# Kernel tuning notes

Hardware: AMD Instinct MI355X
Metric: run time of the kernel (lower is better)

The kernel has to match this reference:

```python
import jax, jax.numpy as jnp
import numpy as np

N_NODES = 100000
N_EDGES = 3200000
NFEAT = 128
NHID = 128
NCLASS = 8
BN_EPS = 1e-5


def setup_inputs() -> dict:
    key = jax.random.key(0)
    ks = jax.random.split(key, 8)
    x = jax.random.normal(ks[0], (N_NODES, NFEAT), dtype=jnp.float32)
    edge_index = jax.random.randint(ks[1], (2, N_EDGES), 0, N_NODES, dtype=jnp.int64)
    # GCNConv params: weight [nfeat, nhid] (glorot), bias [nhid]
    lim = float(np.sqrt(6.0 / (NFEAT + NHID)))
    W = jax.random.uniform(ks[2], (NFEAT, NHID), minval=-lim, maxval=lim, dtype=jnp.float32)
    b_gc = jnp.zeros((NHID,), dtype=jnp.float32)
    # BatchNorm1d params
    gamma = jnp.ones((NHID,), dtype=jnp.float32)
    beta = jnp.zeros((NHID,), dtype=jnp.float32)
    # fc head: (nhid/2) -> nclass, xavier_uniform, zero bias
    lim2 = float(np.sqrt(6.0 / (NHID // 2 + NCLASS)))
    fc_w = jax.random.uniform(ks[3], (NCLASS, NHID // 2), minval=-lim2, maxval=lim2, dtype=jnp.float32)
    fc_b = jnp.zeros((NCLASS,), dtype=jnp.float32)
    return {"x": x, "edge_index": edge_index, "W": W, "b_gc": b_gc,
            "gamma": gamma, "beta": beta, "fc_w": fc_w, "fc_b": fc_b}


def _gcn_conv(x, edge_index, W, b):
    """PyG GCNConv: add self-loops, symmetric norm, linear, gather-scatter, bias."""
    N = x.shape[0]
    loops = jnp.arange(N, dtype=edge_index.dtype)
    src = jnp.concatenate([edge_index[0], loops])  # source (row / x_j)
    dst = jnp.concatenate([edge_index[1], loops])  # target (col / aggregation index)
    # degree of target nodes (edge weight = 1)
    deg = jax.ops.segment_sum(jnp.ones_like(dst, dtype=x.dtype), dst, num_segments=N)
    dinv = jnp.where(deg > 0, jax.lax.rsqrt(deg), 0.0)
    norm = dinv[src] * dinv[dst]  # [E+N]
    h = x @ W  # [N, nhid]
    msg = h[src] * norm[:, None]  # gather + scale
    out = jax.ops.segment_sum(msg, dst, num_segments=N)  # scatter-add
    return out + b


def _batchnorm(h, gamma, beta):
    mean = jnp.mean(h, axis=0)
    var = jnp.mean(jnp.square(h - mean), axis=0)  # biased, training-mode
    return gamma * (h - mean) * jax.lax.rsqrt(var + BN_EPS) + beta


def reference(x, edge_index, W, b_gc, gamma, beta, fc_w, fc_b):
    h = _gcn_conv(x, edge_index, W, b_gc)
    embed = _batchnorm(h, gamma, beta)
    half = embed.shape[1] // 2
    out = embed[:, :half] @ fc_w.T + fc_b
    return (out, embed)
```

## Files before the change

kernel.cpp:

```cpp
#include <hip/hip_runtime.h>
#include <hip/hip_bf16.h>
#include <math.h>

#define N_NODES 100000
#define N_EDGES 3200000
#define NFEAT 128
#define NHID 128
#define NCLASS 8
#define BN_EPS 1e-5f
#define CB 512
#define NBC 196
#define EPB 8192
#define PART_BLOCKS 391
#define WT_BLOCKS 64

typedef __attribute__((ext_vector_type(8))) short short8;
typedef __attribute__((ext_vector_type(4))) float f32x4;

__device__ __forceinline__ short f2bf(float f) {
    __hip_bfloat16 b = __float2bfloat16(f);
    return *reinterpret_cast<short*>(&b);
}
__device__ __forceinline__ float bf_lo(unsigned u) { return __uint_as_float(u << 16); }
__device__ __forceinline__ float bf_hi(unsigned u) { return __uint_as_float(u & 0xffff0000u); }


__global__ __launch_bounds__(256) void k_chist(const int* __restrict__ dst,
                                               int* __restrict__ ghist,
                                               const float* __restrict__ W,
                                               unsigned short* __restrict__ Wt,
                                               uint4* __restrict__ hbz) {
    if (blockIdx.x >= PART_BLOCKS) {
        int idx = (blockIdx.x - PART_BLOCKS) * 256 + threadIdx.x;
        if (idx < 16) hbz[idx] = (uint4){0u, 0u, 0u, 0u};
        int k = idx >> 7, n = idx & 127;
        Wt[n * NFEAT + k] = (unsigned short)f2bf(W[idx]);
        return;
    }
    __shared__ int lh[NBC];
    const int tid = threadIdx.x;
    if (tid < NBC) lh[tid] = 0;
    __syncthreads();
    const int4* dst4 = (const int4*)dst;
    const int q0 = blockIdx.x * (EPB / 4) + tid;
#pragma unroll
    for (int i = 0; i < 8; ++i) {
        int q = q0 + i * 256;
        if (q < N_EDGES / 4) {
            int4 d = dst4[q];
            atomicAdd(&lh[d.x >> 9], 1);
            atomicAdd(&lh[d.y >> 9], 1);
            atomicAdd(&lh[d.z >> 9], 1);
            atomicAdd(&lh[d.w >> 9], 1);
        }
    }
    __syncthreads();
    if (tid < NBC) {
        int c = lh[tid];
        if (c) atomicAdd(&ghist[tid], c);
    }
}

__global__ __launch_bounds__(512) void k_cscan(const int* __restrict__ ghist,
                                               int* __restrict__ coff,
                                               int* __restrict__ ccur,
                                               int* __restrict__ off,
                                               float* __restrict__ stats,
                                               int* __restrict__ ticket) {
    __shared__ int tmp[512];
    const int t = threadIdx.x;
    if (t < 256) stats[t] = 0.f;
    if (t == 0) *ticket = 0;
    int v = (t < NBC) ? ghist[t] : 0;
    tmp[t] = v;
    __syncthreads();
    for (int d = 1; d < 512; d <<= 1) {
        int u = (t >= d) ? tmp[t - d] : 0;
        __syncthreads();
        tmp[t] += u;
        __syncthreads();
    }
    int excl = tmp[t] - v;
    if (t < NBC) {
        coff[t] = excl;
        ccur[t] = excl;
    }
    if (t == NBC - 1) {
        coff[NBC] = tmp[t];
        off[N_NODES] = tmp[t];
    }
}


__global__ __launch_bounds__(256) void k_part(const int* __restrict__ src,
                                              const int* __restrict__ dst,
                                              int* __restrict__ ccur,
                                              unsigned* __restrict__ epack) {
    __shared__ int lh[NBC];
    __shared__ int lstart[NBC];
    __shared__ int adj[NBC];
    __shared__ int stmp[256];
    __shared__ unsigned sorted[EPB];
    __shared__ unsigned short bkt[EPB];
    const int tid = threadIdx.x;
    if (tid < NBC) lh[tid] = 0;
    __syncthreads();
    const int4* src4 = (const int4*)src;
    const int4* dst4 = (const int4*)dst;
    const int q0 = blockIdx.x * (EPB / 4) + tid;
    int4 sv[8], dv[8];
    int rk[32];
#pragma unroll
    for (int i = 0; i < 8; ++i) {
        int q = q0 + i * 256;
        if (q < N_EDGES / 4) {
            sv[i] = src4[q];
            dv[i] = dst4[q];
            rk[i * 4 + 0] = atomicAdd(&lh[dv[i].x >> 9], 1);
            rk[i * 4 + 1] = atomicAdd(&lh[dv[i].y >> 9], 1);
            rk[i * 4 + 2] = atomicAdd(&lh[dv[i].z >> 9], 1);
            rk[i * 4 + 3] = atomicAdd(&lh[dv[i].w >> 9], 1);
        } else dv[i].x = -1;
    }
    __syncthreads();
    int v = (tid < NBC) ? lh[tid] : 0;
    stmp[tid] = v;
    __syncthreads();
    for (int d = 1; d < 256; d <<= 1) {
        int u = (tid >= d) ? stmp[tid - d] : 0;
        __syncthreads();
        stmp[tid] += u;
        __syncthreads();
    }
    if (tid < NBC) {
        int ls = stmp[tid] - v;
        lstart[tid] = ls;
        adj[tid] = (v ? atomicAdd(&ccur[tid], v) : 0) - ls;
    }
    __syncthreads();
#pragma unroll
    for (int i = 0; i < 8; ++i) {
        if (dv[i].x >= 0) {
            int b, p;
            b = dv[i].x >> 9; p = lstart[b] + rk[i * 4 + 0];
            sorted[p] = ((unsigned)sv[i].x << 9) | (unsigned)(dv[i].x & 511); bkt[p] = (unsigned short)b;
            b = dv[i].y >> 9; p = lstart[b] + rk[i * 4 + 1];
            sorted[p] = ((unsigned)sv[i].y << 9) | (unsigned)(dv[i].y & 511); bkt[p] = (unsigned short)b;
            b = dv[i].z >> 9; p = lstart[b] + rk[i * 4 + 2];
            sorted[p] = ((unsigned)sv[i].z << 9) | (unsigned)(dv[i].z & 511); bkt[p] = (unsigned short)b;
            b = dv[i].w >> 9; p = lstart[b] + rk[i * 4 + 3];
            sorted[p] = ((unsigned)sv[i].w << 9) | (unsigned)(dv[i].w & 511); bkt[p] = (unsigned short)b;
        }
    }
    __syncthreads();
    const int vcnt = stmp[255];
    for (int p = tid; p < vcnt; p += 256)
        epack[p + adj[bkt[p]]] = sorted[p];
}


__global__ __launch_bounds__(256) void k_fine(const unsigned* __restrict__ epack,
                                              const int* __restrict__ coff,
                                              int* __restrict__ off,
                                              float* __restrict__ dinv,
                                              int* __restrict__ esrc) {
    __shared__ int lh[CB], lcur[CB], lsc[256];
    const int tid = threadIdx.x;
    const int b = blockIdx.x;
    const int node0 = b << 9;
    lh[tid] = 0;
    lh[tid + 256] = 0;
    __syncthreads();
    const int lo = coff[b], hiEnd = coff[b + 1];
    for (int i = lo + tid; i < hiEnd; i += 256)
        atomicAdd(&lh[epack[i] & 511u], 1);
    __syncthreads();
    int v0 = lh[2 * tid], v1 = lh[2 * tid + 1];
    int s = v0 + v1;
    lsc[tid] = s;
    __syncthreads();
    for (int d = 1; d < 256; d <<= 1) {
        int u = (tid >= d) ? lsc[tid - d] : 0;
        __syncthreads();
        lsc[tid] += u;
        __syncthreads();
    }
    int pairExcl = lsc[tid] - s;
    lcur[2 * tid] = pairExcl;
    lcur[2 * tid + 1] = pairExcl + v0;
    int n0 = node0 + 2 * tid, n1 = n0 + 1;
    if (n0 < N_NODES) { off[n0] = lo + pairExcl;      dinv[n0] = rsqrtf((float)(v0 + 1)); }
    if (n1 < N_NODES) { off[n1] = lo + pairExcl + v0; dinv[n1] = rsqrtf((float)(v1 + 1)); }
    __syncthreads();
    for (int i = lo + tid; i < hiEnd; i += 256) {
        unsigned p = epack[i];
        int pos = atomicAdd(&lcur[p & 511u], 1);
        esrc[lo + pos] = (int)(p >> 9);
    }
}


#define WSTRIDE 136
__global__ __launch_bounds__(256) void k_gemm(const float* __restrict__ x,
                                              const unsigned short* __restrict__ Wt,
                                              const float* __restrict__ dinv,
                                              unsigned short* __restrict__ hb) {
    __shared__ short wlds[NHID * WSTRIDE];
    const int tid = threadIdx.x;

    const unsigned* Wt32 = (const unsigned*)Wt;
    unsigned* wl32 = (unsigned*)wlds;
#pragma unroll
    for (int i = 0; i < 32; ++i) {
        int d = tid + i * 256;
        int n = d >> 6, kp = d & 63;
        wl32[n * (WSTRIDE / 2) + kp] = Wt32[d];
    }
    __syncthreads();

    const int wid = tid >> 6, lane = tid & 63;
    const int qw = lane >> 4, lr = lane & 15;
    const int arow = blockIdx.x * 64 + wid * 16 + lr;
    const bool avalid = arow < N_NODES;

    short8 a[4];
#pragma unroll
    for (int ks = 0; ks < 4; ++ks) {
        if (avalid) {
            const float* p = x + (size_t)arow * NFEAT + ks * 32 + qw * 8;
            float4 v0 = *(const float4*)p;
            float4 v1 = *(const float4*)(p + 4);
            short8 t;
            t[0] = f2bf(v0.x); t[1] = f2bf(v0.y); t[2] = f2bf(v0.z); t[3] = f2bf(v0.w);
            t[4] = f2bf(v1.x); t[5] = f2bf(v1.y); t[6] = f2bf(v1.z); t[7] = f2bf(v1.w);
            a[ks] = t;
        } else {
            short8 t;
#pragma unroll
            for (int j = 0; j < 8; ++j) t[j] = 0;
            a[ks] = t;
        }
    }

    f32x4 acc[8];
#pragma unroll
    for (int nt = 0; nt < 8; ++nt) acc[nt] = (f32x4){0.f, 0.f, 0.f, 0.f};

#pragma unroll
    for (int nt = 0; nt < 8; ++nt) {
#pragma unroll
        for (int ks = 0; ks < 4; ++ks) {
            short8 bfr = *(const short8*)&wlds[(nt * 16 + lr) * WSTRIDE + ks * 32 + qw * 8];
            acc[nt] = __builtin_amdgcn_mfma_f32_16x16x32_bf16(a[ks], bfr, acc[nt], 0, 0, 0);
        }
    }

    const int rbase = blockIdx.x * 64 + wid * 16 + qw * 4;
    float dv[4];
#pragma unroll
    for (int j = 0; j < 4; ++j) dv[j] = (rbase + j < N_NODES) ? dinv[rbase + j] : 0.f;
#pragma unroll
    for (int j = 0; j < 4; ++j) {
        int r = rbase + j;
        if (r >= N_NODES) continue;
#pragma unroll
        for (int nt = 0; nt < 8; ++nt)
            hb[(size_t)r * NHID + nt * 16 + lr] = (unsigned short)f2bf(dv[j] * acc[nt][j]);
    }
}


__global__ __launch_bounds__(256) void k_agg(const int* __restrict__ off,
                                             const int* __restrict__ esrc,
                                             const float* __restrict__ dinv,
                                             const uint2* __restrict__ hbq,
                                             float4* __restrict__ agg4) {
    const int node = (blockIdx.x << 2) | (threadIdx.x >> 6);
    const int lane = threadIdx.x & 63;
    const int hl = lane >> 5;
    const int cl = lane & 31;
    if (node >= N_NODES) return;

    const float dn = dinv[node];
    const int self = hl ? N_NODES : node;
    uint2 u0 = hbq[(size_t)self * 32 + cl];
    float aAx = bf_lo(u0.x), aAy = bf_hi(u0.x), aAz = bf_lo(u0.y), aAw = bf_hi(u0.y);
    float aBx = 0.f, aBy = 0.f, aBz = 0.f, aBw = 0.f;
    float aCx = 0.f, aCy = 0.f, aCz = 0.f, aCw = 0.f;
    float aDx = 0.f, aDy = 0.f, aDz = 0.f, aDw = 0.f;

    const int begin = off[node], end = off[node + 1];
    for (int base = begin; base < end; base += 64) {
        int m = end - base;
        if (m > 64) m = 64;
        int sv = (lane < m) ? esrc[base + lane] : N_NODES;
        const int kmax = (m + 7) >> 3;
        for (int k = 0; k < kmax; ++k) {
            int sA = __shfl(sv, 8 * k + 0 + hl);
            int sB = __shfl(sv, 8 * k + 2 + hl);
            int sC = __shfl(sv, 8 * k + 4 + hl);
            int sD = __shfl(sv, 8 * k + 6 + hl);
            uint2 uA = hbq[(size_t)sA * 32 + cl];
            uint2 uB = hbq[(size_t)sB * 32 + cl];
            uint2 uC = hbq[(size_t)sC * 32 + cl];
            uint2 uD = hbq[(size_t)sD * 32 + cl];
            aAx += bf_lo(uA.x); aAy += bf_hi(uA.x); aAz += bf_lo(uA.y); aAw += bf_hi(uA.y);
            aBx += bf_lo(uB.x); aBy += bf_hi(uB.x); aBz += bf_lo(uB.y); aBw += bf_hi(uB.y);
            aCx += bf_lo(uC.x); aCy += bf_hi(uC.x); aCz += bf_lo(uC.y); aCw += bf_hi(uC.y);
            aDx += bf_lo(uD.x); aDy += bf_hi(uD.x); aDz += bf_lo(uD.y); aDw += bf_hi(uD.y);
        }
    }
    float ax = (aAx + aBx) + (aCx + aDx);
    float ay = (aAy + aBy) + (aCy + aDy);
    float az = (aAz + aBz) + (aCz + aDz);
    float aw = (aAw + aBw) + (aCw + aDw);
    ax += __shfl_xor(ax, 32);
    ay += __shfl_xor(ay, 32);
    az += __shfl_xor(az, 32);
    aw += __shfl_xor(aw, 32);
    if (hl == 0) {
        float4 o;
        o.x = ax * dn; o.y = ay * dn; o.z = az * dn; o.w = aw * dn;
        agg4[(size_t)node * 32 + cl] = o;
    }
}


__global__ __launch_bounds__(256) void k_stats(const float* __restrict__ agg,
                                               float* __restrict__ stats,
                                               int* __restrict__ ticket,
                                               const float* __restrict__ gamma,
                                               const float* __restrict__ beta,
                                               float* __restrict__ ss) {
    const int cb = threadIdx.x & 31;
    const int rg = threadIdx.x >> 5;
    const float4* a4 = (const float4*)agg;
    float4 s = {0.f, 0.f, 0.f, 0.f}, s2 = {0.f, 0.f, 0.f, 0.f};
    for (int r = blockIdx.x * 8 + rg; r < N_NODES; r += gridDim.x * 8) {
        float4 v = a4[(size_t)r * 32 + cb];
        s.x += v.x; s.y += v.y; s.z += v.z; s.w += v.w;
        s2.x += v.x * v.x; s2.y += v.y * v.y; s2.z += v.z * v.z; s2.w += v.w * v.w;
    }
    __shared__ float4 ls[256], ls2[256];
    __shared__ int lastflag;
    ls[threadIdx.x] = s;
    ls2[threadIdx.x] = s2;
    __syncthreads();
    if (rg == 0) {
        float4 ts = ls[cb], t2 = ls2[cb];
#pragma unroll
        for (int g = 1; g < 8; ++g) {
            float4 v = ls[g * 32 + cb], w = ls2[g * 32 + cb];
            ts.x += v.x; ts.y += v.y; ts.z += v.z; ts.w += v.w;
            t2.x += w.x; t2.y += w.y; t2.z += w.z; t2.w += w.w;
        }
        atomicAdd(&stats[cb * 4 + 0], ts.x);
        atomicAdd(&stats[cb * 4 + 1], ts.y);
        atomicAdd(&stats[cb * 4 + 2], ts.z);
        atomicAdd(&stats[cb * 4 + 3], ts.w);
        atomicAdd(&stats[128 + cb * 4 + 0], t2.x);
        atomicAdd(&stats[128 + cb * 4 + 1], t2.y);
        atomicAdd(&stats[128 + cb * 4 + 2], t2.z);
        atomicAdd(&stats[128 + cb * 4 + 3], t2.w);
    }
    __threadfence();
    __syncthreads();
    if (threadIdx.x == 0)
        lastflag = (atomicAdd(ticket, 1) == (int)gridDim.x - 1) ? 1 : 0;
    __syncthreads();
    if (lastflag && threadIdx.x < NHID) {
        int c = threadIdx.x;
        float sum = atomicAdd(&stats[c], 0.f);
        float sq  = atomicAdd(&stats[128 + c], 0.f);
        float mean = sum / (float)N_NODES;
        float var = fmaxf(sq / (float)N_NODES - mean * mean, 0.f);
        float inv = rsqrtf(var + BN_EPS);
        float sc = gamma[c] * inv;
        ss[c] = sc;
        ss[128 + c] = beta[c] - mean * sc;
    }
}


__global__ __launch_bounds__(256) void k_bnfc(float* __restrict__ embed,
                                              const float* __restrict__ ss,
                                              const float* __restrict__ fc_w,
                                              const float* __restrict__ fc_b,
                                              float* __restrict__ out) {
    __shared__ float se[64][68];
    __shared__ float sw[8][68];
    __shared__ float sb[8];
    const int tid = threadIdx.x;
    const int row0 = blockIdx.x * 64;
    {
        int d = tid;
        sw[d >> 6][d & 63] = fc_w[d];
        d = tid + 256;
        sw[d >> 6][d & 63] = fc_w[d];
        if (tid < 8) sb[tid] = fc_b[tid];
    }
    float4* ef4 = (float4*)embed;
    const float4* ssc4 = (const float4*)ss;
    const float4* ssh4 = (const float4*)(ss + 128);
#pragma unroll
    for (int i = 0; i < 8; ++i) {
        int d = tid + i * 256;
        int r = d >> 5;
        int cb = d & 31;
        int gr = row0 + r;
        if (gr < N_NODES) {
            float4 v = ef4[(size_t)gr * 32 + cb];
            float4 sc = ssc4[cb], sh = ssh4[cb];
            v.x = fmaf(v.x, sc.x, sh.x);
            v.y = fmaf(v.y, sc.y, sh.y);
            v.z = fmaf(v.z, sc.z, sh.z);
            v.w = fmaf(v.w, sc.w, sh.w);
            ef4[(size_t)gr * 32 + cb] = v;
            if (cb < 16) {
                se[r][cb * 4 + 0] = v.x; se[r][cb * 4 + 1] = v.y;
                se[r][cb * 4 + 2] = v.z; se[r][cb * 4 + 3] = v.w;
            }
        } else if (cb < 16) {
            se[r][cb * 4 + 0] = 0.f; se[r][cb * 4 + 1] = 0.f;
            se[r][cb * 4 + 2] = 0.f; se[r][cb * 4 + 3] = 0.f;
        }
    }
    __syncthreads();
    const int r = tid >> 2;
    const int j0 = (tid & 3) * 2;
    const int gr = row0 + r;
#pragma unroll
    for (int jj = 0; jj < 2; ++jj) {
        int j = j0 + jj;
        float s = sb[j];
#pragma unroll
        for (int k = 0; k < 64; ++k) s = fmaf(se[r][k], sw[j][k], s);
        if (gr < N_NODES) out[(size_t)gr * NCLASS + j] = s;
    }
}


extern "C" void kernel_launch(void* const* d_in, const int* in_sizes, int n_in,
                              void* d_out, int out_size, void* d_ws, size_t ws_size,
                              hipStream_t stream) {
    const float* x     = (const float*)d_in[0];
    const int*   ei    = (const int*)d_in[1];
    const float* W     = (const float*)d_in[2];
    const float* gamma = (const float*)d_in[4];
    const float* beta  = (const float*)d_in[5];
    const float* fc_w  = (const float*)d_in[6];
    const float* fc_b  = (const float*)d_in[7];

    const int* src = ei;
    const int* dst = ei + N_EDGES;

    float* out   = (float*)d_out;
    float* embed = (float*)d_out + (size_t)N_NODES * NCLASS;

    char* ws = (char*)d_ws;
    size_t o = 0;
    unsigned* epack = (unsigned*)(ws + o);          o += (size_t)N_EDGES * 4;
    unsigned short* hb = (unsigned short*)(ws + o); o += (size_t)(N_NODES + 1) * NHID * 2;
    o = (o + 255) & ~(size_t)255;
    int* esrc   = (int*)(ws + o);                   o += (size_t)N_EDGES * 4;
    int* off    = (int*)(ws + o);                   o += (size_t)(N_NODES + 1) * 4;
    float* dinv = (float*)(ws + o);                 o += (size_t)N_NODES * 4;
    unsigned short* Wt = (unsigned short*)(ws + o); o += (size_t)NFEAT * NHID * 2;
    float* stats = (float*)(ws + o);                o += 256 * 4;
    float* ss    = (float*)(ws + o);                o += 256 * 4;
    int* ghist   = (int*)(ws + o);                  o += NBC * 4;
    int* coff    = (int*)(ws + o);                  o += (NBC + 1) * 4;
    int* ccur    = (int*)(ws + o);                  o += NBC * 4;
    int* ticket  = (int*)(ws + o);                  o += 4;

    hipMemsetAsync(ghist, 0, NBC * 4, stream);

    k_chist<<<PART_BLOCKS + WT_BLOCKS, 256, 0, stream>>>(dst, ghist, W, Wt,
                                                         (uint4*)(hb + (size_t)N_NODES * NHID));
    k_cscan<<<1, 512, 0, stream>>>(ghist, coff, ccur, off, stats, ticket);
    k_part<<<PART_BLOCKS, 256, 0, stream>>>(src, dst, ccur, epack);
    k_fine<<<NBC, 256, 0, stream>>>(epack, coff, off, dinv, esrc);

    k_gemm<<<(N_NODES + 63) / 64, 256, 0, stream>>>(x, Wt, dinv, hb);

    k_agg<<<(N_NODES + 3) / 4, 256, 0, stream>>>(off, esrc, dinv, (const uint2*)hb, (float4*)embed);

    k_stats<<<512, 256, 0, stream>>>(embed, stats, ticket, gamma, beta, ss);

    k_bnfc<<<(N_NODES + 63) / 64, 256, 0, stream>>>(embed, ss, fc_w, fc_b, out);
}
```

Baseline: 314.3 us.

## Fuse BN statistics into aggregation kernel and stage x through LDS in GEMM

The aggregation kernel becomes persistent-style, with 2048 blocks looping over groups of four nodes. It accumulates per-column sums and sums of squares while writing each output row, then reduces them per block and does the last-block ticket finalize, so the separate stats kernel and its re-read of the 100000x128 fp32 buffer go away. The GEMM now loads x tiles into padded LDS with coalesced float4 loads before forming MFMA fragments, in place of per-lane strided global loads. In exchange the aggregation grid is smaller, which may reduce latency hiding for the irregular gathers, and the GEMM uses more shared memory per block.

```diff
diff --git a/kernel.cpp b/kernel.cpp
--- a/kernel.cpp
+++ b/kernel.cpp
@@ -13,6 +13,8 @@
 #define EPB 8192
 #define PART_BLOCKS 391
 #define WT_BLOCKS 64
+#define AGG_BLOCKS 2048
+#define NODE_GROUPS (N_NODES / 4)
 
 typedef __attribute__((ext_vector_type(8))) short short8;
 typedef __attribute__((ext_vector_type(4))) float f32x4;
@@ -201,12 +203,15 @@
 
 
 #define WSTRIDE 136
+#define XSTRIDE 136
 __global__ __launch_bounds__(256) void k_gemm(const float* __restrict__ x,
                                               const unsigned short* __restrict__ Wt,
                                               const float* __restrict__ dinv,
                                               unsigned short* __restrict__ hb) {
-    __shared__ short wlds[NHID * WSTRIDE];
+    __shared__ __align__(16) short wlds[NHID * WSTRIDE];
+    __shared__ __align__(16) short xl[64 * XSTRIDE];
     const int tid = threadIdx.x;
+    const int row0 = blockIdx.x * 64;
 
     const unsigned* Wt32 = (const unsigned*)Wt;
     unsigned* wl32 = (unsigned*)wlds;
@@ -216,31 +221,27 @@
         int n = d >> 6, kp = d & 63;
         wl32[n * (WSTRIDE / 2) + kp] = Wt32[d];
     }
+    const float4* x4 = (const float4*)x;
+#pragma unroll
+    for (int i = 0; i < 8; ++i) {
+        int idx = tid + i * 256;
+        int r = idx >> 5, c4 = idx & 31;
+        int gr = row0 + r;
+        float4 vv = (gr < N_NODES) ? x4[(size_t)gr * 32 + c4]
+                                   : (float4){0.f, 0.f, 0.f, 0.f};
+        short4 t;
+        t.x = f2bf(vv.x); t.y = f2bf(vv.y); t.z = f2bf(vv.z); t.w = f2bf(vv.w);
+        *(short4*)&xl[r * XSTRIDE + c4 * 4] = t;
+    }
     __syncthreads();
 
     const int wid = tid >> 6, lane = tid & 63;
     const int qw = lane >> 4, lr = lane & 15;
-    const int arow = blockIdx.x * 64 + wid * 16 + lr;
-    const bool avalid = arow < N_NODES;
 
     short8 a[4];
 #pragma unroll
-    for (int ks = 0; ks < 4; ++ks) {
-        if (avalid) {
-            const float* p = x + (size_t)arow * NFEAT + ks * 32 + qw * 8;
-            float4 v0 = *(const float4*)p;
-            float4 v1 = *(const float4*)(p + 4);
-            short8 t;
-            t[0] = f2bf(v0.x); t[1] = f2bf(v0.y); t[2] = f2bf(v0.z); t[3] = f2bf(v0.w);
-            t[4] = f2bf(v1.x); t[5] = f2bf(v1.y); t[6] = f2bf(v1.z); t[7] = f2bf(v1.w);
-            a[ks] = t;
-        } else {
-            short8 t;
-#pragma unroll
-            for (int j = 0; j < 8; ++j) t[j] = 0;
-            a[ks] = t;
-        }
-    }
+    for (int ks = 0; ks < 4; ++ks)
+        a[ks] = *(const short8*)&xl[(wid * 16 + lr) * XSTRIDE + ks * 32 + qw * 8];
 
     f32x4 acc[8];
 #pragma unroll
@@ -274,99 +275,95 @@
                                              const int* __restrict__ esrc,
                                              const float* __restrict__ dinv,
                                              const uint2* __restrict__ hbq,
-                                             float4* __restrict__ agg4) {
-    const int node = (blockIdx.x << 2) | (threadIdx.x >> 6);
+                                             float4* __restrict__ agg4,
+                                             float* __restrict__ stats,
+                                             int* __restrict__ ticket,
+                                             const float* __restrict__ gamma,
+                                             const float* __restrict__ beta,
+                                             float* __restrict__ ss) {
+    const int wv = threadIdx.x >> 6;
     const int lane = threadIdx.x & 63;
     const int hl = lane >> 5;
     const int cl = lane & 31;
-    if (node >= N_NODES) return;
-
-    const float dn = dinv[node];
-    const int self = hl ? N_NODES : node;
-    uint2 u0 = hbq[(size_t)self * 32 + cl];
-    float aAx = bf_lo(u0.x), aAy = bf_hi(u0.x), aAz = bf_lo(u0.y), aAw = bf_hi(u0.y);
-    float aBx = 0.f, aBy = 0.f, aBz = 0.f, aBw = 0.f;
-    float aCx = 0.f, aCy = 0.f, aCz = 0.f, aCw = 0.f;
-    float aDx = 0.f, aDy = 0.f, aDz = 0.f, aDw = 0.f;
-
-    const int begin = off[node], end = off[node + 1];
-    for (int base = begin; base < end; base += 64) {
-        int m = end - base;
-        if (m > 64) m = 64;
-        int sv = (lane < m) ? esrc[base + lane] : N_NODES;
-        const int kmax = (m + 7) >> 3;
-        for (int k = 0; k < kmax; ++k) {
-            int sA = __shfl(sv, 8 * k + 0 + hl);
-            int sB = __shfl(sv, 8 * k + 2 + hl);
-            int sC = __shfl(sv, 8 * k + 4 + hl);
-            int sD = __shfl(sv, 8 * k + 6 + hl);
-            uint2 uA = hbq[(size_t)sA * 32 + cl];
-            uint2 uB = hbq[(size_t)sB * 32 + cl];
-            uint2 uC = hbq[(size_t)sC * 32 + cl];
-            uint2 uD = hbq[(size_t)sD * 32 + cl];
-            aAx += bf_lo(uA.x); aAy += bf_hi(uA.x); aAz += bf_lo(uA.y); aAw += bf_hi(uA.y);
-            aBx += bf_lo(uB.x); aBy += bf_hi(uB.x); aBz += bf_lo(uB.y); aBw += bf_hi(uB.y);
-            aCx += bf_lo(uC.x); aCy += bf_hi(uC.x); aCz += bf_lo(uC.y); aCw += bf_hi(uC.y);
-            aDx += bf_lo(uD.x); aDy += bf_hi(uD.x); aDz += bf_lo(uD.y); aDw += bf_hi(uD.y);
-        }
-    }
-    float ax = (aAx + aBx) + (aCx + aDx);
-    float ay = (aAy + aBy) + (aCy + aDy);
-    float az = (aAz + aBz) + (aCz + aDz);
-    float aw = (aAw + aBw) + (aCw + aDw);
-    ax += __shfl_xor(ax, 32);
-    ay += __shfl_xor(ay, 32);
-    az += __shfl_xor(az, 32);
-    aw += __shfl_xor(aw, 32);
+
+    float4 sAcc = {0.f, 0.f, 0.f, 0.f}, qAcc = {0.f, 0.f, 0.f, 0.f};
+
+    for (int ng = blockIdx.x; ng < NODE_GROUPS; ng += AGG_BLOCKS) {
+        const int node = ng * 4 + wv;
+        const float dn = dinv[node];
+        const int self = hl ? N_NODES : node;
+        uint2 u0 = hbq[(size_t)self * 32 + cl];
+        float aAx = bf_lo(u0.x), aAy = bf_hi(u0.x), aAz = bf_lo(u0.y), aAw = bf_hi(u0.y);
+        float aBx = 0.f, aBy = 0.f, aBz = 0.f, aBw = 0.f;
+        float aCx = 0.f, aCy = 0.f, aCz = 0.f, aCw = 0.f;
+        float aDx = 0.f, aDy = 0.f, aDz = 0.f, aDw = 0.f;
+
+        const int begin = off[node], end = off[node + 1];
+        for (int base = begin; base < end; base += 64) {
+            int m = end - base;
+            if (m > 64) m = 64;
+            int sv = (lane < m) ? esrc[base + lane] : N_NODES;
+            const int kmax = (m + 7) >> 3;
+            for (int k = 0; k < kmax; ++k) {
+                int sA = __shfl(sv, 8 * k + 0 + hl);
+                int sB = __shfl(sv, 8 * k + 2 + hl);
+                int sC = __shfl(sv, 8 * k + 4 + hl);
+                int sD = __shfl(sv, 8 * k + 6 + hl);
+                uint2 uA = hbq[(size_t)sA * 32 + cl];
+                uint2 uB = hbq[(size_t)sB * 32 + cl];
+                uint2 uC = hbq[(size_t)sC * 32 + cl];
+                uint2 uD = hbq[(size_t)sD * 32 + cl];
+                aAx += bf_lo(uA.x); aAy += bf_hi(uA.x); aAz += bf_lo(uA.y); aAw += bf_hi(uA.y);
+                aBx += bf_lo(uB.x); aBy += bf_hi(uB.x); aBz += bf_lo(uB.y); aBw += bf_hi(uB.y);
+                aCx += bf_lo(uC.x); aCy += bf_hi(uC.x); aCz += bf_lo(uC.y); aCw += bf_hi(uC.y);
+                aDx += bf_lo(uD.x); aDy += bf_hi(uD.x); aDz += bf_lo(uD.y); aDw += bf_hi(uD.y);
+            }
+        }
+        float ax = (aAx + aBx) + (aCx + aDx);
+        float ay = (aAy + aBy) + (aCy + aDy);
+        float az = (aAz + aBz) + (aCz + aDz);
+        float aw = (aAw + aBw) + (aCw + aDw);
+        ax += __shfl_xor(ax, 32);
+        ay += __shfl_xor(ay, 32);
+        az += __shfl_xor(az, 32);
+        aw += __shfl_xor(aw, 32);
+        if (hl == 0) {
+            float4 o;
+            o.x = ax * dn; o.y = ay * dn; o.z = az * dn; o.w = aw * dn;
+            agg4[(size_t)node * 32 + cl] = o;
+            sAcc.x += o.x; sAcc.y += o.y; sAcc.z += o.z; sAcc.w += o.w;
+            qAcc.x += o.x * o.x; qAcc.y += o.y * o.y; qAcc.z += o.z * o.z; qAcc.w += o.w * o.w;
+        }
+    }
+
+    __shared__ float4 lsS[128], lsQ[128];
+    __shared__ int lastflag;
     if (hl == 0) {
-        float4 o;
-        o.x = ax * dn; o.y = ay * dn; o.z = az * dn; o.w = aw * dn;
-        agg4[(size_t)node * 32 + cl] = o;
-    }
-}
-
-
-__global__ __launch_bounds__(256) void k_stats(const float* __restrict__ agg,
-                                               float* __restrict__ stats,
-                                               int* __restrict__ ticket,
-                                               const float* __restrict__ gamma,
-                                               const float* __restrict__ beta,
-                                               float* __restrict__ ss) {
-    const int cb = threadIdx.x & 31;
-    const int rg = threadIdx.x >> 5;
-    const float4* a4 = (const float4*)agg;
-    float4 s = {0.f, 0.f, 0.f, 0.f}, s2 = {0.f, 0.f, 0.f, 0.f};
-    for (int r = blockIdx.x * 8 + rg; r < N_NODES; r += gridDim.x * 8) {
-        float4 v = a4[(size_t)r * 32 + cb];
-        s.x += v.x; s.y += v.y; s.z += v.z; s.w += v.w;
-        s2.x += v.x * v.x; s2.y += v.y * v.y; s2.z += v.z * v.z; s2.w += v.w * v.w;
-    }
-    __shared__ float4 ls[256], ls2[256];
-    __shared__ int lastflag;
-    ls[threadIdx.x] = s;
-    ls2[threadIdx.x] = s2;
-    __syncthreads();
-    if (rg == 0) {
-        float4 ts = ls[cb], t2 = ls2[cb];
-#pragma unroll
-        for (int g = 1; g < 8; ++g) {
-            float4 v = ls[g * 32 + cb], w = ls2[g * 32 + cb];
-            ts.x += v.x; ts.y += v.y; ts.z += v.z; ts.w += v.w;
-            t2.x += w.x; t2.y += w.y; t2.z += w.z; t2.w += w.w;
-        }
-        atomicAdd(&stats[cb * 4 + 0], ts.x);
-        atomicAdd(&stats[cb * 4 + 1], ts.y);
-        atomicAdd(&stats[cb * 4 + 2], ts.z);
-        atomicAdd(&stats[cb * 4 + 3], ts.w);
-        atomicAdd(&stats[128 + cb * 4 + 0], t2.x);
-        atomicAdd(&stats[128 + cb * 4 + 1], t2.y);
-        atomicAdd(&stats[128 + cb * 4 + 2], t2.z);
-        atomicAdd(&stats[128 + cb * 4 + 3], t2.w);
+        lsS[wv * 32 + cl] = sAcc;
+        lsQ[wv * 32 + cl] = qAcc;
+    }
+    __syncthreads();
+    if (threadIdx.x < 32) {
+        float4 ts = lsS[threadIdx.x], tq = lsQ[threadIdx.x];
+#pragma unroll
+        for (int g = 1; g < 4; ++g) {
+            float4 a = lsS[g * 32 + threadIdx.x], b = lsQ[g * 32 + threadIdx.x];
+            ts.x += a.x; ts.y += a.y; ts.z += a.z; ts.w += a.w;
+            tq.x += b.x; tq.y += b.y; tq.z += b.z; tq.w += b.w;
+        }
+        atomicAdd(&stats[threadIdx.x * 4 + 0], ts.x);
+        atomicAdd(&stats[threadIdx.x * 4 + 1], ts.y);
+        atomicAdd(&stats[threadIdx.x * 4 + 2], ts.z);
+        atomicAdd(&stats[threadIdx.x * 4 + 3], ts.w);
+        atomicAdd(&stats[128 + threadIdx.x * 4 + 0], tq.x);
+        atomicAdd(&stats[128 + threadIdx.x * 4 + 1], tq.y);
+        atomicAdd(&stats[128 + threadIdx.x * 4 + 2], tq.z);
+        atomicAdd(&stats[128 + threadIdx.x * 4 + 3], tq.w);
     }
     __threadfence();
     __syncthreads();
     if (threadIdx.x == 0)
-        lastflag = (atomicAdd(ticket, 1) == (int)gridDim.x - 1) ? 1 : 0;
+        lastflag = (atomicAdd(ticket, 1) == AGG_BLOCKS - 1) ? 1 : 0;
     __syncthreads();
     if (lastflag && threadIdx.x < NHID) {
         int c = threadIdx.x;
@@ -483,9 +480,8 @@
 
     k_gemm<<<(N_NODES + 63) / 64, 256, 0, stream>>>(x, Wt, dinv, hb);
 
-    k_agg<<<(N_NODES + 3) / 4, 256, 0, stream>>>(off, esrc, dinv, (const uint2*)hb, (float4*)embed);
-
-    k_stats<<<512, 256, 0, stream>>>(embed, stats, ticket, gamma, beta, ss);
+    k_agg<<<AGG_BLOCKS, 256, 0, stream>>>(off, esrc, dinv, (const uint2*)hb, (float4*)embed,
+                                          stats, ticket, gamma, beta, ss);
 
     k_bnfc<<<(N_NODES + 63) / 64, 256, 0, stream>>>(embed, ss, fc_w, fc_b, out);
 }
```

Result: slower. 485.9 us (+54.6%).
